# Performance work log

Hardware: AMD Instinct MI355X
Metric: run time of the kernel (lower is better)

Reference implementation:

```python
import jax, jax.numpy as jnp
import numpy as np

P = 399   # number of unshared per-position Conv1d kernels
K = 5     # conv kernel width (padding=2, 'same')


def _conv_stage(x, W, b):
    """Locally-connected stage: a distinct Conv1d per position along the last axis.
    x: [B, Cin, T, P]; W: [P, Cout, Cin, K]; b: [P, Cout] -> [B, Cout, T, P]."""
    xt = jnp.transpose(x, (3, 0, 1, 2))  # [P, B, Cin, T]

    def one(xi, wi, bi):
        y = jax.lax.conv_general_dilated(xi, wi, (1,), [(2, 2)],
                                         dimension_numbers=('NCH', 'OIH', 'NCH'))
        return y + bi[None, :, None]

    y = jax.vmap(one)(xt, W, b)          # [P, B, Cout, T]
    return jnp.transpose(y, (1, 2, 3, 0))


def _maxpool(x):
    # MaxPool2d((10,1), stride=(3,1)) over [B, C, T, P]
    return jax.lax.reduce_window(x, -jnp.inf, jax.lax.max,
                                 (1, 1, 10, 1), (1, 1, 3, 1), 'VALID')


def setup_inputs() -> dict:
    key = jax.random.key(0)
    ks = jax.random.split(key, 32)
    B, T = 256, 365

    def rn(k, shape, scale):
        return jax.random.normal(k, shape, jnp.float32) * scale

    d = {}
    d['x'] = jax.random.normal(ks[0], (B, T, P), jnp.float32)
    d['x2'] = jax.random.normal(ks[1], (B, 1307), jnp.float32)
    # per-position conv weights (PyTorch Conv1d layout O,I,K, stacked over P)
    d['W1'] = rn(ks[2], (P, 3, 1, K), 0.3); d['b1'] = rn(ks[3], (P, 3), 0.05)
    d['W2'] = rn(ks[4], (P, 3, 3, K), 0.2); d['b2'] = rn(ks[5], (P, 3), 0.05)
    d['W3'] = rn(ks[6], (P, 3, 3, K), 0.2); d['b3'] = rn(ks[7], (P, 3), 0.05)
    d['W4'] = rn(ks[8], (P, 3, 3, K), 0.2); d['b4'] = rn(ks[9], (P, 3), 0.05)
    # self.layers: 1307 -> 700 -> 200 -> 100
    d['lW1'] = rn(ks[10], (1307, 700), 0.02); d['lb1'] = rn(ks[11], (700,), 0.01)
    d['lW2'] = rn(ks[12], (700, 200), 0.03);  d['lb2'] = rn(ks[13], (200,), 0.01)
    d['lW3'] = rn(ks[14], (200, 100), 0.05);  d['lb3'] = rn(ks[15], (100,), 0.01)
    # self.common_layers: 1297 -> 500 -> 100 -> 20
    d['cW1'] = rn(ks[16], (1297, 500), 0.02); d['cb1'] = rn(ks[17], (500,), 0.01)
    d['cW2'] = rn(ks[18], (500, 100), 0.04);  d['cb2'] = rn(ks[19], (100,), 0.01)
    d['cW3'] = rn(ks[20], (100, 20), 0.08);   d['cb3'] = rn(ks[21], (20,), 0.01)
    # last_layer: 20 -> 1
    d['fW'] = rn(ks[22], (20, 1), 0.2);       d['fb'] = rn(ks[23], (1,), 0.01)
    return d


def reference(x, x2, W1, b1, W2, b2, W3, b3, W4, b4,
              lW1, lb1, lW2, lb2, lW3, lb3,
              cW1, cb1, cW2, cb2, cW3, cb3, fW, fb):
    h = x[:, None, :, :]                       # [B, 1, T, P]
    for W, b in ((W1, b1), (W2, b2), (W3, b3), (W4, b4)):
        h = _maxpool(jax.nn.relu(_conv_stage(h, W, b)))
    enc1 = h.reshape(h.shape[0], -1)           # [B, 3*1*399] = [B, 1197]

    e = jax.nn.relu(x2 @ lW1 + lb1)
    e = jax.nn.relu(e @ lW2 + lb2)
    enc2 = e @ lW3 + lb3                       # [B, 100] (no ReLU on final Linear)

    c = jnp.concatenate([enc1, enc2], axis=1)  # [B, 1297]
    c = jax.nn.relu(c @ cW1 + cb1)
    c = jax.nn.relu(c @ cW2 + cb2)
    c = jax.nn.relu(c @ cW3 + cb3)
    return c @ fW + fb                         # [B, 1]
```

## Files before the change

kernel.cpp:

```cpp
#include <hip/hip_runtime.h>

#define PP 399
#define BB 256


template<int SEG>
__device__ __forceinline__ float xload(const float* __restrict__ inp, int idx) {
    if (SEG == 2) {
        int ic = idx < 364 ? idx : 364;
        float v = inp[(long)ic * PP];
        return (idx <= 364) ? v : 0.f;
    }
    return inp[(long)idx * PP];
}

template<int OFF>
__device__ __forceinline__ void s1_group(const float (&xv)[13],
    const float (&w1)[3][5], const float (&B1)[3],
    float (&A1)[3], float (&c0)[3])
{
#pragma unroll
    for (int co = 0; co < 3; ++co) {
        float a0 = B1[co], a1 = B1[co], a2 = B1[co];
#pragma unroll
        for (int t = 0; t < 5; ++t) {
            a0 = fmaf(xv[OFF + t],     w1[co][t], a0);
            a1 = fmaf(xv[OFF + 1 + t], w1[co][t], a1);
            a2 = fmaf(xv[OFF + 2 + t], w1[co][t], a2);
        }
        c0[co] = a0;
        A1[co] = fmaxf(fmaxf(a0, a1), a2);
    }
}

template<int P2>
__device__ __forceinline__ void s2_step(
    float (&fe)[3][4], const float (&e)[3],
    const float (&w2)[3][3][5], const float (&B2)[3],
    float (&A2a)[3], float (&A2b)[3], float (&A2c)[3], float (&A2cur)[3],
    float*& op, bool do_c2, bool do_emit)
{
    if (do_c2) {
        float c2v[3];
#pragma unroll
        for (int co = 0; co < 3; ++co) {
            float a = B2[co];
#pragma unroll
            for (int ci = 0; ci < 3; ++ci) {
                a = fmaf(fe[ci][0], w2[co][ci][0], a);
                a = fmaf(fe[ci][1], w2[co][ci][1], a);
                a = fmaf(fe[ci][2], w2[co][ci][2], a);
                a = fmaf(fe[ci][3], w2[co][ci][3], a);
                a = fmaf(e[ci],     w2[co][ci][4], a);
            }
            c2v[co] = a;
        }
        if (P2 == 0) {
#pragma unroll
            for (int co = 0; co < 3; ++co) { A2a[co] = A2b[co]; A2b[co] = A2c[co]; A2c[co] = A2cur[co]; }
            if (do_emit) {
#pragma unroll
                for (int co = 0; co < 3; ++co)
                    op[co * PP] = fmaxf(fmaxf(fmaxf(fmaxf(A2a[co], A2b[co]), A2c[co]), c2v[co]), 0.f);
                op += 3 * PP;
            }
#pragma unroll
            for (int co = 0; co < 3; ++co) A2cur[co] = c2v[co];
        } else {
#pragma unroll
            for (int co = 0; co < 3; ++co) A2cur[co] = fmaxf(A2cur[co], c2v[co]);
        }
    }
#pragma unroll
    for (int ci = 0; ci < 3; ++ci) {
        fe[ci][0] = fe[ci][1]; fe[ci][1] = fe[ci][2]; fe[ci][2] = fe[ci][3]; fe[ci][3] = e[ci];
    }
}

template<int P2>
__device__ __forceinline__ void emit_e(
    const float (&Aa)[3], const float (&Ab)[3], const float (&Ac)[3],
    const float (&c0)[3],
    float (&fe)[3][4],
    const float (&w2)[3][3][5], const float (&B2)[3],
    float (&A2a)[3], float (&A2b)[3], float (&A2c)[3], float (&A2cur)[3],
    float*& op, bool do_c2, bool do_emit)
{
    float e[3];
#pragma unroll
    for (int co = 0; co < 3; ++co)
        e[co] = fmaxf(fmaxf(fmaxf(fmaxf(Aa[co], Ab[co]), Ac[co]), c0[co]), 0.f);
    s2_step<P2>(fe, e, w2, B2, A2a, A2b, A2c, A2cur, op, do_c2, do_emit);
}

template<int SEG>
__device__ __forceinline__ void s12_body(
    const float* __restrict__ x,
    const float* __restrict__ W1, const float* __restrict__ b1,
    const float* __restrict__ W2, const float* __restrict__ b2,
    float* __restrict__ h2, int b, int p)
{
    constexpr int J0tab[4] = {0, 13, 25, 37};
    constexpr int j0 = J0tab[SEG];
    constexpr int j1 = J0tab[SEG + 1];
    constexpr int k0 = (SEG == 0) ? 0 : 3 * j0 - 2;
    constexpr int kend = (3 * j1 + 11 < 121) ? (3 * j1 + 11) : 121;
    constexpr int NGRP = kend - k0 + 1;
    constexpr int NS = NGRP / 3;
    constexpr int NREM = NGRP - 3 * NS;
    constexpr int c2start = (SEG == 0) ? 5 : (k0 + 7);
    constexpr int e2start = 3 * j0 + 14;
    constexpr int P2_0 = (SEG == 0) ? 1 : 2;
    constexpr int P2_1 = (SEG == 0) ? 2 : 0;
    constexpr int P2_2 = (SEG == 0) ? 0 : 1;

    float w1[3][5], B1[3];
    {
        const float* wp = W1 + (long)p * 15;
#pragma unroll
        for (int co = 0; co < 3; ++co) {
#pragma unroll
            for (int t = 0; t < 5; ++t) w1[co][t] = wp[co * 5 + t];
            B1[co] = b1[(long)p * 3 + co];
        }
    }
    float w2[3][3][5], B2[3];
    {
        const float* wp = W2 + (long)p * 45;
#pragma unroll
        for (int co = 0; co < 3; ++co) {
#pragma unroll
            for (int ci = 0; ci < 3; ++ci)
#pragma unroll
                for (int t = 0; t < 5; ++t) w2[co][ci][t] = wp[(co * 3 + ci) * 5 + t];
            B2[co] = b2[(long)p * 3 + co];
        }
    }

    const float* __restrict__ inp = x + (long)b * 365 * PP + p;
    float* op = h2 + ((long)b * 37 + j0) * 3 * PP + p;

    float xv[13];
#pragma unroll
    for (int s = 0; s < 13; ++s) {
        int idx = 3 * k0 - 2 + s;
        xv[s] = (idx >= 0) ? inp[(long)idx * PP] : 0.f;
    }

    float fe[3][4];
    float A1p[3][3];
    float A2a[3], A2b[3], A2c[3], A2cur[3];
#pragma unroll
    for (int ci = 0; ci < 3; ++ci)
#pragma unroll
        for (int s = 0; s < 4; ++s) fe[ci][s] = 0.f;
#pragma unroll
    for (int co = 0; co < 3; ++co) {
        A1p[0][co] = 0.f; A1p[1][co] = 0.f; A1p[2][co] = 0.f;
        A2a[co] = 0.f; A2b[co] = 0.f; A2c[co] = 0.f; A2cur[co] = 0.f;
    }

    for (int S = 0; S < NS; ++S) {
        int k = k0 + 3 * S;
        float q[9];
#pragma unroll
        for (int s = 0; s < 9; ++s)
            q[s] = xload<SEG>(inp, 3 * k + 11 + s);

        float A1c0[3], A1c1[3], A1c2[3], c0[3];

        s1_group<0>(xv, w1, B1, A1c0, c0);
        if (S >= 1)
            emit_e<P2_0>(A1p[0], A1p[1], A1p[2], c0, fe, w2, B2,
                         A2a, A2b, A2c, A2cur, op,
                         k >= c2start, k >= e2start);
        s1_group<3>(xv, w1, B1, A1c1, c0);
        if (S >= 1)
            emit_e<P2_1>(A1p[1], A1p[2], A1c0, c0, fe, w2, B2,
                         A2a, A2b, A2c, A2cur, op,
                         k + 1 >= c2start, k + 1 >= e2start);
        s1_group<6>(xv, w1, B1, A1c2, c0);
        if (S >= 1)
            emit_e<P2_2>(A1p[2], A1c0, A1c1, c0, fe, w2, B2,
                         A2a, A2b, A2c, A2cur, op,
                         k + 2 >= c2start, k + 2 >= e2start);

#pragma unroll
        for (int co = 0; co < 3; ++co) {
            A1p[0][co] = A1c0[co]; A1p[1][co] = A1c1[co]; A1p[2][co] = A1c2[co];
        }
        xv[0] = xv[9]; xv[1] = xv[10]; xv[2] = xv[11]; xv[3] = xv[12];
#pragma unroll
        for (int s = 0; s < 9; ++s) xv[4 + s] = q[s];
    }

    if constexpr (NREM >= 1) {
        int k = k0 + 3 * NS;
        float A1c0[3], c0[3];
        s1_group<0>(xv, w1, B1, A1c0, c0);
        emit_e<P2_0>(A1p[0], A1p[1], A1p[2], c0, fe, w2, B2,
                     A2a, A2b, A2c, A2cur, op,
                     k >= c2start, k >= e2start);
        if constexpr (NREM >= 2) {
            float A1c1[3];
            s1_group<3>(xv, w1, B1, A1c1, c0);
            emit_e<P2_1>(A1p[1], A1p[2], A1c0, c0, fe, w2, B2,
                         A2a, A2b, A2c, A2cur, op,
                         k + 1 >= c2start, k + 1 >= e2start);
        }
    }
    if constexpr (SEG == 2) {
        float ez[3] = {0.f, 0.f, 0.f};
        s2_step<0>(fe, ez, w2, B2, A2a, A2b, A2c, A2cur, op, true, true);
    }
}

template<int RELU_A>
__device__ __forceinline__ void gemm_tile(
    const float* __restrict__ A, const float* __restrict__ Wt,
    float* __restrict__ out, int K, int N, int lda, int ldo, int kchunk,
    int bx, int by, int bz)
{
    __shared__ float As[32][36];
    __shared__ float Bs[32][36];

    int tid = threadIdx.x;
    int ty  = tid >> 3;
    int tx4 = (tid & 7) * 4;
    int c0 = bx * 32;
    int m0 = by * 32;
    int k0 = bz * kchunk;
    int klim = min(K, k0 + kchunk);

    float4 acc = make_float4(0.f, 0.f, 0.f, 0.f);

    for (int kb = k0; kb < klim; kb += 32) {
#pragma unroll
        for (int j = 0; j < 4; ++j) {
            int kk = kb + tx4 + j;
            float v = (kk < klim) ? A[(long)(m0 + ty) * lda + kk] : 0.f;
            if (RELU_A) v = fmaxf(v, 0.f);
            As[ty][tx4 + j] = v;
        }
#pragma unroll
        for (int j = 0; j < 4; ++j) {
            int kk = kb + ty;
            int c = c0 + tx4 + j;
            Bs[ty][tx4 + j] = (kk < klim && c < N) ? Wt[(long)kk * N + c] : 0.f;
        }
        __syncthreads();
#pragma unroll
        for (int kk = 0; kk < 32; ++kk) {
            float a = As[ty][kk];
            float4 bv = *(const float4*)&Bs[kk][tx4];
            acc.x = fmaf(a, bv.x, acc.x);
            acc.y = fmaf(a, bv.y, acc.y);
            acc.z = fmaf(a, bv.z, acc.z);
            acc.w = fmaf(a, bv.w, acc.w);
        }
        __syncthreads();
    }

    long m = m0 + ty;
    if (c0 + tx4 + 0 < N) atomicAdd(&out[m * ldo + c0 + tx4 + 0], acc.x);
    if (c0 + tx4 + 1 < N) atomicAdd(&out[m * ldo + c0 + tx4 + 1], acc.y);
    if (c0 + tx4 + 2 < N) atomicAdd(&out[m * ldo + c0 + tx4 + 2], acc.z);
    if (c0 + tx4 + 3 < N) atomicAdd(&out[m * ldo + c0 + tx4 + 3], acc.w);
}

template<int RELU_A>
__global__ __launch_bounds__(256)
void gemm_atomic(const float* __restrict__ A, const float* __restrict__ Wt,
                 float* __restrict__ out, int K, int N, int lda, int ldo, int kchunk)
{
    gemm_tile<RELU_A>(A, Wt, out, K, N, lda, ldo, kchunk,
                      blockIdx.x, blockIdx.y, blockIdx.z);
}

__global__ __launch_bounds__(256)
void d1_conv_s12_lw1(const float* __restrict__ x,
                     const float* __restrict__ W1, const float* __restrict__ b1,
                     const float* __restrict__ W2, const float* __restrict__ b2,
                     float* __restrict__ h2,
                     const float* __restrict__ x2, const float* __restrict__ lW1,
                     float* __restrict__ e1)
{
    int blk = blockIdx.x;
    if (blk < 1197) {
        int seg = blk / 399;
        int bx  = blk - seg * 399;
        int gid = bx * 256 + threadIdx.x;
        int b = gid / PP;
        int p = gid - b * PP;
        if (seg == 0)      s12_body<0>(x, W1, b1, W2, b2, h2, b, p);
        else if (seg == 1) s12_body<1>(x, W1, b1, W2, b2, h2, b, p);
        else               s12_body<2>(x, W1, b1, W2, b2, h2, b, p);
    } else {
        int g = blk - 1197;
        int gx = g % 22;
        int gy = (g / 22) % 8;
        int gz = g / 176;
        gemm_tile<0>(x2, lW1, e1, 1307, 700, 1307, 700, 256, gx, gy, gz);
    }
}

template<int CIN>
struct Stage {
    float w[3][CIN][5];
    float b[3];
    float xw[CIN][5];
    float m1[3], m2[3], m3[3];
    int nin;
};

__device__ __forceinline__ void init_s3(Stage<3>& s, const float* __restrict__ Wt,
                                        const float* __restrict__ Bs, int p) {
    const float* wp = Wt + (long)p * 45;
#pragma unroll
    for (int co = 0; co < 3; ++co)
#pragma unroll
        for (int ci = 0; ci < 3; ++ci)
#pragma unroll
            for (int k = 0; k < 5; ++k)
                s.w[co][ci][k] = wp[(co * 3 + ci) * 5 + k];
#pragma unroll
    for (int co = 0; co < 3; ++co) s.b[co] = Bs[(long)p * 3 + co];
#pragma unroll
    for (int ci = 0; ci < 3; ++ci)
#pragma unroll
        for (int k = 0; k < 5; ++k) s.xw[ci][k] = 0.f;
#pragma unroll
    for (int co = 0; co < 3; ++co) { s.m1[co] = -1e30f; s.m2[co] = -1e30f; s.m3[co] = -1e30f; }
    s.nin = 0;
}

template<int CIN>
__device__ __forceinline__ bool feed(Stage<CIN>& s, const float* in, float* out) {
#pragma unroll
    for (int ci = 0; ci < CIN; ++ci) {
        s.xw[ci][0] = s.xw[ci][1];
        s.xw[ci][1] = s.xw[ci][2];
        s.xw[ci][2] = s.xw[ci][3];
        s.xw[ci][3] = s.xw[ci][4];
        s.xw[ci][4] = in[ci];
    }
    int t = s.nin - 2;
    s.nin++;
    if (t < 0) return false;

    float c[3];
#pragma unroll
    for (int co = 0; co < 3; ++co) {
        float a = s.b[co];
#pragma unroll
        for (int ci = 0; ci < CIN; ++ci)
#pragma unroll
            for (int k = 0; k < 5; ++k)
                a = fmaf(s.xw[ci][k], s.w[co][ci][k], a);
        c[co] = fmaxf(a, 0.f);
    }

    bool emit = false;
    int ph = t % 3;
    if (ph == 0) {
        if (t >= 9) {
#pragma unroll
            for (int co = 0; co < 3; ++co) out[co] = fmaxf(s.m1[co], c[co]);
            emit = true;
        }
#pragma unroll
        for (int co = 0; co < 3; ++co) {
            float a = fmaxf(s.m2[co], c[co]);
            float bb = fmaxf(s.m3[co], c[co]);
            s.m1[co] = a; s.m2[co] = bb; s.m3[co] = c[co];
        }
    } else {
#pragma unroll
        for (int co = 0; co < 3; ++co) {
            s.m1[co] = fmaxf(s.m1[co], c[co]);
            s.m2[co] = fmaxf(s.m2[co], c[co]);
            s.m3[co] = fmaxf(s.m3[co], c[co]);
        }
    }
    return emit;
}

__device__ __forceinline__ void s34_body(
    const float* __restrict__ h2,
    const float* __restrict__ W3, const float* __restrict__ b3,
    const float* __restrict__ W4, const float* __restrict__ b4,
    float* __restrict__ cbuf, int b, int p)
{
    Stage<3> s3, s4;
    init_s3(s3, W3, b3, p);
    init_s3(s4, W4, b4, p);

    const float* inp = h2 + (long)b * 37 * 3 * PP + p;
    float* o4 = cbuf + (long)b * 1297 + p;

    float v3[3], v4[3];
    float z[3] = {0.f, 0.f, 0.f};

    float r0[3], r1[3], r2[3], r3[3], r4[3];
#pragma unroll
    for (int ci = 0; ci < 3; ++ci) {
        r0[ci] = inp[(long)(0 * 3 + ci) * PP];
        r1[ci] = inp[(long)(1 * 3 + ci) * PP];
        r2[ci] = inp[(long)(2 * 3 + ci) * PP];
        r3[ci] = inp[(long)(3 * 3 + ci) * PP];
        r4[ci] = inp[(long)(4 * 3 + ci) * PP];
    }

    for (int i = 0; i < 39; ++i) {
        float nn[3];
        int i5 = i + 5;
#pragma unroll
        for (int ci = 0; ci < 3; ++ci)
            nn[ci] = (i5 < 37) ? inp[(long)(i5 * 3 + ci) * PP] : 0.f;
        if (feed(s3, r0, v3)) {
            if (feed(s4, v3, v4)) {
#pragma unroll
                for (int co = 0; co < 3; ++co) o4[co * PP] = v4[co];
            }
        }
#pragma unroll
        for (int ci = 0; ci < 3; ++ci) {
            r0[ci] = r1[ci]; r1[ci] = r2[ci]; r2[ci] = r3[ci]; r3[ci] = r4[ci]; r4[ci] = nn[ci];
        }
    }
    for (int r = 0; r < 2; ++r) {
        if (feed(s4, z, v4)) {
#pragma unroll
            for (int co = 0; co < 3; ++co) o4[co * PP] = v4[co];
        }
    }
}

__global__ __launch_bounds__(256)
void d2_conv_s34_lw2(const float* __restrict__ h2,
                     const float* __restrict__ W3, const float* __restrict__ b3,
                     const float* __restrict__ W4, const float* __restrict__ b4,
                     float* __restrict__ cbuf,
                     const float* __restrict__ e1, const float* __restrict__ lW2,
                     float* __restrict__ e2)
{
    int blk = blockIdx.x;
    if (blk < 399) {
        int gid = blk * 256 + threadIdx.x;
        int b = gid / PP;
        int p = gid - b * PP;
        s34_body(h2, W3, b3, W4, b4, cbuf, b, p);
    } else {
        int g = blk - 399;
        int gx = g % 7;
        int gy = (g / 7) % 8;
        int gz = g / 56;
        gemm_tile<1>(e1, lW2, e2, 700, 200, 700, 200, 128, gx, gy, gz);
    }
}

__global__ __launch_bounds__(256)
void init_bias(float* __restrict__ e1, const float* __restrict__ lb1,
               float* __restrict__ e2, const float* __restrict__ lb2,
               float* __restrict__ enc2, const float* __restrict__ lb3,
               float* __restrict__ c1, const float* __restrict__ cb1,
               float* __restrict__ c2, const float* __restrict__ cb2,
               float* __restrict__ c3, const float* __restrict__ cb3)
{
    int idx = blockIdx.x * 256 + threadIdx.x;
    if (idx < BB * 700) { e1[idx] = lb1[idx % 700]; return; }
    idx -= BB * 700;
    if (idx < BB * 200) { e2[idx] = lb2[idx % 200]; return; }
    idx -= BB * 200;
    if (idx < BB * 100) { int m = idx / 100, c = idx % 100; enc2[(long)m * 1297 + c] = lb3[c]; return; }
    idx -= BB * 100;
    if (idx < BB * 500) { c1[idx] = cb1[idx % 500]; return; }
    idx -= BB * 500;
    if (idx < BB * 100) { c2[idx] = cb2[idx % 100]; return; }
    idx -= BB * 100;
    if (idx < BB * 20)  { c3[idx] = cb3[idx % 20]; return; }
}

__global__ __launch_bounds__(64)
void final_kernel(const float* __restrict__ c3,
                  const float* __restrict__ fW,
                  const float* __restrict__ fb,
                  float* __restrict__ out)
{
    int m = blockIdx.x * 64 + threadIdx.x;
    if (m >= BB) return;
    float acc = fb[0];
#pragma unroll
    for (int k = 0; k < 20; ++k)
        acc = fmaf(fmaxf(c3[m * 20 + k], 0.f), fW[k], acc);
    out[m] = acc;
}

extern "C" void kernel_launch(void* const* d_in, const int* in_sizes, int n_in,
                              void* d_out, int out_size, void* d_ws, size_t ws_size,
                              hipStream_t stream)
{
    const float* x   = (const float*)d_in[0];
    const float* x2  = (const float*)d_in[1];
    const float* W1  = (const float*)d_in[2];
    const float* b1  = (const float*)d_in[3];
    const float* W2  = (const float*)d_in[4];
    const float* b2  = (const float*)d_in[5];
    const float* W3  = (const float*)d_in[6];
    const float* b3  = (const float*)d_in[7];
    const float* W4  = (const float*)d_in[8];
    const float* b4  = (const float*)d_in[9];
    const float* lW1 = (const float*)d_in[10];
    const float* lb1 = (const float*)d_in[11];
    const float* lW2 = (const float*)d_in[12];
    const float* lb2 = (const float*)d_in[13];
    const float* lW3 = (const float*)d_in[14];
    const float* lb3 = (const float*)d_in[15];
    const float* cW1 = (const float*)d_in[16];
    const float* cb1 = (const float*)d_in[17];
    const float* cW2 = (const float*)d_in[18];
    const float* cb2 = (const float*)d_in[19];
    const float* cW3 = (const float*)d_in[20];
    const float* cb3 = (const float*)d_in[21];
    const float* fW  = (const float*)d_in[22];
    const float* fb  = (const float*)d_in[23];
    float* out = (float*)d_out;

    float* ws = (float*)d_ws;
    const long n_h2   = (long)BB * 37 * 3 * PP;
    const long n_cbuf = (long)BB * 1297;
    float* h2   = ws;
    float* cbuf = h2 + n_h2;
    float* e1   = cbuf + n_cbuf;
    float* e2   = e1 + (long)BB * 700;
    float* c1   = e2 + (long)BB * 200;
    float* c2   = c1 + (long)BB * 500;
    float* c3b  = c2 + (long)BB * 100;

    init_bias<<<1620, 256, 0, stream>>>(e1, lb1, e2, lb2, cbuf + 1197, lb3,
                                        c1, cb1, c2, cb2, c3b, cb3);

    d1_conv_s12_lw1<<<1197 + 1056, 256, 0, stream>>>(x, W1, b1, W2, b2, h2,
                                                     x2, lW1, e1);
    d2_conv_s34_lw2<<<399 + 336, 256, 0, stream>>>(h2, W3, b3, W4, b4, cbuf,
                                                   e1, lW2, e2);
    gemm_atomic<1><<<dim3(4, 8, 4), 256, 0, stream>>>(e2, lW3, cbuf + 1197, 200, 100, 200, 1297, 64);

    gemm_atomic<0><<<dim3(16, 8, 6), 256, 0, stream>>>(cbuf, cW1, c1, 1297, 500, 1297, 500, 256);
    gemm_atomic<1><<<dim3( 4, 8, 8), 256, 0, stream>>>(c1, cW2, c2, 500, 100, 500, 100, 64);
    gemm_atomic<1><<<dim3( 1, 8, 4), 256, 0, stream>>>(c2, cW3, c3b, 100, 20, 100, 20, 32);

    final_kernel<<<dim3(4), 64, 0, stream>>>(c3b, fW, fb, out);
}
```

Baseline: 161.6 us.

## Process two batch rows per thread and split conv stages into six time segments

The fused stage-1/2 conv kernel now has each thread handle two batch samples (b and b+128), so the per-position weights loaded into registers are reused across two independent streams and there is more instruction-level parallelism. The time axis is split into six segments instead of three, which keeps the block count roughly the same (1200 vs 1197). The cost is roughly double the register pressure for the per-thread state, which may reduce occupancy or cause spills, plus more halo recomputation at the extra segment boundaries.

```diff
diff --git a/kernel.cpp b/kernel.cpp
--- a/kernel.cpp
+++ b/kernel.cpp
@@ -6,7 +6,7 @@
 
 template<int SEG>
 __device__ __forceinline__ float xload(const float* __restrict__ inp, int idx) {
-    if (SEG == 2) {
+    if (SEG == 5) {
         int ic = idx < 364 ? idx : 364;
         float v = inp[(long)ic * PP];
         return (idx <= 364) ? v : 0.f;
@@ -15,92 +15,112 @@
 }
 
 template<int OFF>
-__device__ __forceinline__ void s1_group(const float (&xv)[13],
+__device__ __forceinline__ void s1g2(const float (&xv)[2][13],
     const float (&w1)[3][5], const float (&B1)[3],
-    float (&A1)[3], float (&c0)[3])
-{
-#pragma unroll
-    for (int co = 0; co < 3; ++co) {
-        float a0 = B1[co], a1 = B1[co], a2 = B1[co];
-#pragma unroll
-        for (int t = 0; t < 5; ++t) {
-            a0 = fmaf(xv[OFF + t],     w1[co][t], a0);
-            a1 = fmaf(xv[OFF + 1 + t], w1[co][t], a1);
-            a2 = fmaf(xv[OFF + 2 + t], w1[co][t], a2);
-        }
-        c0[co] = a0;
-        A1[co] = fmaxf(fmaxf(a0, a1), a2);
-    }
+    float (&A1)[2][3], float (&c0)[2][3])
+{
+#pragma unroll
+    for (int st = 0; st < 2; ++st)
+#pragma unroll
+        for (int co = 0; co < 3; ++co) {
+            float a0 = B1[co], a1 = B1[co], a2 = B1[co];
+#pragma unroll
+            for (int t = 0; t < 5; ++t) {
+                a0 = fmaf(xv[st][OFF + t],     w1[co][t], a0);
+                a1 = fmaf(xv[st][OFF + 1 + t], w1[co][t], a1);
+                a2 = fmaf(xv[st][OFF + 2 + t], w1[co][t], a2);
+            }
+            c0[st][co] = a0;
+            A1[st][co] = fmaxf(fmaxf(a0, a1), a2);
+        }
 }
 
 template<int P2>
-__device__ __forceinline__ void s2_step(
-    float (&fe)[3][4], const float (&e)[3],
+__device__ __forceinline__ void s2s2(
+    float (&fe)[2][3][4], const float (&e)[2][3],
     const float (&w2)[3][3][5], const float (&B2)[3],
-    float (&A2a)[3], float (&A2b)[3], float (&A2c)[3], float (&A2cur)[3],
-    float*& op, bool do_c2, bool do_emit)
+    float (&A2a)[2][3], float (&A2b)[2][3], float (&A2c)[2][3], float (&A2cur)[2][3],
+    float* (&op)[2], bool do_c2, bool do_emit)
 {
     if (do_c2) {
-        float c2v[3];
-#pragma unroll
-        for (int co = 0; co < 3; ++co) {
-            float a = B2[co];
-#pragma unroll
-            for (int ci = 0; ci < 3; ++ci) {
-                a = fmaf(fe[ci][0], w2[co][ci][0], a);
-                a = fmaf(fe[ci][1], w2[co][ci][1], a);
-                a = fmaf(fe[ci][2], w2[co][ci][2], a);
-                a = fmaf(fe[ci][3], w2[co][ci][3], a);
-                a = fmaf(e[ci],     w2[co][ci][4], a);
+        float c2v[2][3];
+#pragma unroll
+        for (int st = 0; st < 2; ++st)
+#pragma unroll
+            for (int co = 0; co < 3; ++co) {
+                float a = B2[co];
+#pragma unroll
+                for (int ci = 0; ci < 3; ++ci) {
+                    a = fmaf(fe[st][ci][0], w2[co][ci][0], a);
+                    a = fmaf(fe[st][ci][1], w2[co][ci][1], a);
+                    a = fmaf(fe[st][ci][2], w2[co][ci][2], a);
+                    a = fmaf(fe[st][ci][3], w2[co][ci][3], a);
+                    a = fmaf(e[st][ci],     w2[co][ci][4], a);
+                }
+                c2v[st][co] = a;
             }
-            c2v[co] = a;
-        }
         if (P2 == 0) {
 #pragma unroll
-            for (int co = 0; co < 3; ++co) { A2a[co] = A2b[co]; A2b[co] = A2c[co]; A2c[co] = A2cur[co]; }
+            for (int st = 0; st < 2; ++st)
+#pragma unroll
+                for (int co = 0; co < 3; ++co) {
+                    A2a[st][co] = A2b[st][co]; A2b[st][co] = A2c[st][co]; A2c[st][co] = A2cur[st][co];
+                }
             if (do_emit) {
 #pragma unroll
-                for (int co = 0; co < 3; ++co)
-                    op[co * PP] = fmaxf(fmaxf(fmaxf(fmaxf(A2a[co], A2b[co]), A2c[co]), c2v[co]), 0.f);
-                op += 3 * PP;
+                for (int st = 0; st < 2; ++st) {
+#pragma unroll
+                    for (int co = 0; co < 3; ++co)
+                        op[st][co * PP] = fmaxf(fmaxf(fmaxf(fmaxf(A2a[st][co], A2b[st][co]), A2c[st][co]), c2v[st][co]), 0.f);
+                    op[st] += 3 * PP;
+                }
             }
 #pragma unroll
-            for (int co = 0; co < 3; ++co) A2cur[co] = c2v[co];
+            for (int st = 0; st < 2; ++st)
+#pragma unroll
+                for (int co = 0; co < 3; ++co) A2cur[st][co] = c2v[st][co];
         } else {
 #pragma unroll
-            for (int co = 0; co < 3; ++co) A2cur[co] = fmaxf(A2cur[co], c2v[co]);
-        }
-    }
-#pragma unroll
-    for (int ci = 0; ci < 3; ++ci) {
-        fe[ci][0] = fe[ci][1]; fe[ci][1] = fe[ci][2]; fe[ci][2] = fe[ci][3]; fe[ci][3] = e[ci];
-    }
+            for (int st = 0; st < 2; ++st)
+#pragma unroll
+                for (int co = 0; co < 3; ++co) A2cur[st][co] = fmaxf(A2cur[st][co], c2v[st][co]);
+        }
+    }
+#pragma unroll
+    for (int st = 0; st < 2; ++st)
+#pragma unroll
+        for (int ci = 0; ci < 3; ++ci) {
+            fe[st][ci][0] = fe[st][ci][1]; fe[st][ci][1] = fe[st][ci][2];
+            fe[st][ci][2] = fe[st][ci][3]; fe[st][ci][3] = e[st][ci];
+        }
 }
 
 template<int P2>
-__device__ __forceinline__ void emit_e(
-    const float (&Aa)[3], const float (&Ab)[3], const float (&Ac)[3],
-    const float (&c0)[3],
-    float (&fe)[3][4],
+__device__ __forceinline__ void emit2(
+    const float (&Aa)[2][3], const float (&Ab)[2][3], const float (&Ac)[2][3],
+    const float (&c0)[2][3],
+    float (&fe)[2][3][4],
     const float (&w2)[3][3][5], const float (&B2)[3],
-    float (&A2a)[3], float (&A2b)[3], float (&A2c)[3], float (&A2cur)[3],
-    float*& op, bool do_c2, bool do_emit)
-{
-    float e[3];
-#pragma unroll
-    for (int co = 0; co < 3; ++co)
-        e[co] = fmaxf(fmaxf(fmaxf(fmaxf(Aa[co], Ab[co]), Ac[co]), c0[co]), 0.f);
-    s2_step<P2>(fe, e, w2, B2, A2a, A2b, A2c, A2cur, op, do_c2, do_emit);
+    float (&A2a)[2][3], float (&A2b)[2][3], float (&A2c)[2][3], float (&A2cur)[2][3],
+    float* (&op)[2], bool do_c2, bool do_emit)
+{
+    float e[2][3];
+#pragma unroll
+    for (int st = 0; st < 2; ++st)
+#pragma unroll
+        for (int co = 0; co < 3; ++co)
+            e[st][co] = fmaxf(fmaxf(fmaxf(fmaxf(Aa[st][co], Ab[st][co]), Ac[st][co]), c0[st][co]), 0.f);
+    s2s2<P2>(fe, e, w2, B2, A2a, A2b, A2c, A2cur, op, do_c2, do_emit);
 }
 
 template<int SEG>
-__device__ __forceinline__ void s12_body(
+__device__ __forceinline__ void s12_dual(
     const float* __restrict__ x,
     const float* __restrict__ W1, const float* __restrict__ b1,
     const float* __restrict__ W2, const float* __restrict__ b2,
     float* __restrict__ h2, int b, int p)
 {
-    constexpr int J0tab[4] = {0, 13, 25, 37};
+    constexpr int J0tab[7] = {0, 7, 13, 19, 25, 31, 37};
     constexpr int j0 = J0tab[SEG];
     constexpr int j1 = J0tab[SEG + 1];
     constexpr int k0 = (SEG == 0) ? 0 : 3 * j0 - 2;
@@ -137,81 +157,94 @@
         }
     }
 
-    const float* __restrict__ inp = x + (long)b * 365 * PP + p;
-    float* op = h2 + ((long)b * 37 + j0) * 3 * PP + p;
-
-    float xv[13];
-#pragma unroll
-    for (int s = 0; s < 13; ++s) {
-        int idx = 3 * k0 - 2 + s;
-        xv[s] = (idx >= 0) ? inp[(long)idx * PP] : 0.f;
-    }
-
-    float fe[3][4];
-    float A1p[3][3];
-    float A2a[3], A2b[3], A2c[3], A2cur[3];
-#pragma unroll
-    for (int ci = 0; ci < 3; ++ci)
-#pragma unroll
-        for (int s = 0; s < 4; ++s) fe[ci][s] = 0.f;
-#pragma unroll
-    for (int co = 0; co < 3; ++co) {
-        A1p[0][co] = 0.f; A1p[1][co] = 0.f; A1p[2][co] = 0.f;
-        A2a[co] = 0.f; A2b[co] = 0.f; A2c[co] = 0.f; A2cur[co] = 0.f;
+    const float* inp[2] = { x + (long)b * 365 * PP + p,
+                            x + (long)(b + 128) * 365 * PP + p };
+    float* op[2] = { h2 + ((long)b * 37 + j0) * 3 * PP + p,
+                     h2 + ((long)(b + 128) * 37 + j0) * 3 * PP + p };
+
+    float xv[2][13];
+#pragma unroll
+    for (int st = 0; st < 2; ++st)
+#pragma unroll
+        for (int s = 0; s < 13; ++s) {
+            int idx = 3 * k0 - 2 + s;
+            xv[st][s] = (idx >= 0) ? inp[st][(long)idx * PP] : 0.f;
+        }
+
+    float fe[2][3][4];
+    float A1p0[2][3], A1p1[2][3], A1p2[2][3];
+    float A2a[2][3], A2b[2][3], A2c[2][3], A2cur[2][3];
+#pragma unroll
+    for (int st = 0; st < 2; ++st) {
+#pragma unroll
+        for (int ci = 0; ci < 3; ++ci)
+#pragma unroll
+            for (int s = 0; s < 4; ++s) fe[st][ci][s] = 0.f;
+#pragma unroll
+        for (int co = 0; co < 3; ++co) {
+            A1p0[st][co] = 0.f; A1p1[st][co] = 0.f; A1p2[st][co] = 0.f;
+            A2a[st][co] = 0.f; A2b[st][co] = 0.f; A2c[st][co] = 0.f; A2cur[st][co] = 0.f;
+        }
     }
 
     for (int S = 0; S < NS; ++S) {
         int k = k0 + 3 * S;
-        float q[9];
-#pragma unroll
-        for (int s = 0; s < 9; ++s)
-            q[s] = xload<SEG>(inp, 3 * k + 11 + s);
-
-        float A1c0[3], A1c1[3], A1c2[3], c0[3];
-
-        s1_group<0>(xv, w1, B1, A1c0, c0);
+        float q[2][9];
+#pragma unroll
+        for (int st = 0; st < 2; ++st)
+#pragma unroll
+            for (int s = 0; s < 9; ++s)
+                q[st][s] = xload<SEG>(inp[st], 3 * k + 11 + s);
+
+        float A1c0[2][3], A1c1[2][3], A1c2[2][3], c0[2][3];
+
+        s1g2<0>(xv, w1, B1, A1c0, c0);
         if (S >= 1)
-            emit_e<P2_0>(A1p[0], A1p[1], A1p[2], c0, fe, w2, B2,
-                         A2a, A2b, A2c, A2cur, op,
-                         k >= c2start, k >= e2start);
-        s1_group<3>(xv, w1, B1, A1c1, c0);
+            emit2<P2_0>(A1p0, A1p1, A1p2, c0, fe, w2, B2,
+                        A2a, A2b, A2c, A2cur, op,
+                        k >= c2start, k >= e2start);
+        s1g2<3>(xv, w1, B1, A1c1, c0);
         if (S >= 1)
-            emit_e<P2_1>(A1p[1], A1p[2], A1c0, c0, fe, w2, B2,
-                         A2a, A2b, A2c, A2cur, op,
-                         k + 1 >= c2start, k + 1 >= e2start);
-        s1_group<6>(xv, w1, B1, A1c2, c0);
+            emit2<P2_1>(A1p1, A1p2, A1c0, c0, fe, w2, B2,
+                        A2a, A2b, A2c, A2cur, op,
+                        k + 1 >= c2start, k + 1 >= e2start);
+        s1g2<6>(xv, w1, B1, A1c2, c0);
         if (S >= 1)
-            emit_e<P2_2>(A1p[2], A1c0, A1c1, c0, fe, w2, B2,
-                         A2a, A2b, A2c, A2cur, op,
-                         k + 2 >= c2start, k + 2 >= e2start);
-
-#pragma unroll
-        for (int co = 0; co < 3; ++co) {
-            A1p[0][co] = A1c0[co]; A1p[1][co] = A1c1[co]; A1p[2][co] = A1c2[co];
-        }
-        xv[0] = xv[9]; xv[1] = xv[10]; xv[2] = xv[11]; xv[3] = xv[12];
-#pragma unroll
-        for (int s = 0; s < 9; ++s) xv[4 + s] = q[s];
+            emit2<P2_2>(A1p2, A1c0, A1c1, c0, fe, w2, B2,
+                        A2a, A2b, A2c, A2cur, op,
+                        k + 2 >= c2start, k + 2 >= e2start);
+
+#pragma unroll
+        for (int st = 0; st < 2; ++st) {
+#pragma unroll
+            for (int co = 0; co < 3; ++co) {
+                A1p0[st][co] = A1c0[st][co]; A1p1[st][co] = A1c1[st][co]; A1p2[st][co] = A1c2[st][co];
+            }
+            xv[st][0] = xv[st][9]; xv[st][1] = xv[st][10];
+            xv[st][2] = xv[st][11]; xv[st][3] = xv[st][12];
+#pragma unroll
+            for (int s = 0; s < 9; ++s) xv[st][4 + s] = q[st][s];
+        }
     }
 
     if constexpr (NREM >= 1) {
         int k = k0 + 3 * NS;
-        float A1c0[3], c0[3];
-        s1_group<0>(xv, w1, B1, A1c0, c0);
-        emit_e<P2_0>(A1p[0], A1p[1], A1p[2], c0, fe, w2, B2,
-                     A2a, A2b, A2c, A2cur, op,
-                     k >= c2start, k >= e2start);
+        float A1c0[2][3], c0[2][3];
+        s1g2<0>(xv, w1, B1, A1c0, c0);
+        emit2<P2_0>(A1p0, A1p1, A1p2, c0, fe, w2, B2,
+                    A2a, A2b, A2c, A2cur, op,
+                    k >= c2start, k >= e2start);
         if constexpr (NREM >= 2) {
-            float A1c1[3];
-            s1_group<3>(xv, w1, B1, A1c1, c0);
-            emit_e<P2_1>(A1p[1], A1p[2], A1c0, c0, fe, w2, B2,
-                         A2a, A2b, A2c, A2cur, op,
-                         k + 1 >= c2start, k + 1 >= e2start);
-        }
-    }
-    if constexpr (SEG == 2) {
-        float ez[3] = {0.f, 0.f, 0.f};
-        s2_step<0>(fe, ez, w2, B2, A2a, A2b, A2c, A2cur, op, true, true);
+            float A1c1[2][3];
+            s1g2<3>(xv, w1, B1, A1c1, c0);
+            emit2<P2_1>(A1p1, A1p2, A1c0, c0, fe, w2, B2,
+                        A2a, A2b, A2c, A2cur, op,
+                        k + 1 >= c2start, k + 1 >= e2start);
+        }
+    }
+    if constexpr (SEG == 5) {
+        float ez[2][3] = {{0.f, 0.f, 0.f}, {0.f, 0.f, 0.f}};
+        s2s2<0>(fe, ez, w2, B2, A2a, A2b, A2c, A2cur, op, true, true);
     }
 }
 
@@ -286,17 +319,23 @@
                      float* __restrict__ e1)
 {
     int blk = blockIdx.x;
-    if (blk < 1197) {
-        int seg = blk / 399;
-        int bx  = blk - seg * 399;
+    if (blk < 1200) {
+        int seg = blk / 200;
+        int bx  = blk - seg * 200;
         int gid = bx * 256 + threadIdx.x;
+        if (gid >= 128 * PP) return;
         int b = gid / PP;
         int p = gid - b * PP;
-        if (seg == 0)      s12_body<0>(x, W1, b1, W2, b2, h2, b, p);
-        else if (seg == 1) s12_body<1>(x, W1, b1, W2, b2, h2, b, p);
-        else               s12_body<2>(x, W1, b1, W2, b2, h2, b, p);
+        switch (seg) {
+            case 0: s12_dual<0>(x, W1, b1, W2, b2, h2, b, p); break;
+            case 1: s12_dual<1>(x, W1, b1, W2, b2, h2, b, p); break;
+            case 2: s12_dual<2>(x, W1, b1, W2, b2, h2, b, p); break;
+            case 3: s12_dual<3>(x, W1, b1, W2, b2, h2, b, p); break;
+            case 4: s12_dual<4>(x, W1, b1, W2, b2, h2, b, p); break;
+            default: s12_dual<5>(x, W1, b1, W2, b2, h2, b, p); break;
+        }
     } else {
-        int g = blk - 1197;
+        int g = blk - 1200;
         int gx = g % 22;
         int gy = (g / 22) % 8;
         int gz = g / 176;
@@ -540,7 +579,7 @@
     init_bias<<<1620, 256, 0, stream>>>(e1, lb1, e2, lb2, cbuf + 1197, lb3,
                                         c1, cb1, c2, cb2, c3b, cb3);
 
-    d1_conv_s12_lw1<<<1197 + 1056, 256, 0, stream>>>(x, W1, b1, W2, b2, h2,
+    d1_conv_s12_lw1<<<1200 + 1056, 256, 0, stream>>>(x, W1, b1, W2, b2, h2,
                                                      x2, lW1, e1);
     d2_conv_s34_lw2<<<399 + 336, 256, 0, stream>>>(h2, W3, b3, W4, b4, cbuf,
                                                    e1, lW2, e2);
```

New measurement: 228.7 us. +41.6%, slower.

## Fold bias init into conv launch and overlap cW1 enc1 part with lW3 GEMM

Applied to the files above, without the earlier changes.

Only e1's bias init stays as a standalone kernel; the other bias buffers are now filled by extra blocks appended to the first conv/GEMM launch. The cW1 GEMM is split by K range: its enc1 part (first 1197 rows) runs in the same launch as the lW3 GEMM, since it does not depend on enc2. A small follow-up launch then handles the remaining 100 rows that come from enc2. The aim is to shorten the serial chain of small kernels and fill the GPU better, at the cost of more complex block dispatch.

```diff
diff --git a/kernel.cpp b/kernel.cpp
--- a/kernel.cpp
+++ b/kernel.cpp
@@ -278,12 +278,24 @@
 }
 
 __global__ __launch_bounds__(256)
+void init_e1(float* __restrict__ e1, const float* __restrict__ lb1)
+{
+    int idx = blockIdx.x * 256 + threadIdx.x;
+    if (idx < BB * 700) e1[idx] = lb1[idx % 700];
+}
+
+__global__ __launch_bounds__(256)
 void d1_conv_s12_lw1(const float* __restrict__ x,
                      const float* __restrict__ W1, const float* __restrict__ b1,
                      const float* __restrict__ W2, const float* __restrict__ b2,
                      float* __restrict__ h2,
                      const float* __restrict__ x2, const float* __restrict__ lW1,
-                     float* __restrict__ e1)
+                     float* __restrict__ e1,
+                     float* __restrict__ e2,  const float* __restrict__ lb2,
+                     float* __restrict__ cbuf, const float* __restrict__ lb3,
+                     float* __restrict__ c1,  const float* __restrict__ cb1,
+                     float* __restrict__ c2,  const float* __restrict__ cb2,
+                     float* __restrict__ c3b, const float* __restrict__ cb3)
 {
     int blk = blockIdx.x;
     if (blk < 1197) {
@@ -295,12 +307,23 @@
         if (seg == 0)      s12_body<0>(x, W1, b1, W2, b2, h2, b, p);
         else if (seg == 1) s12_body<1>(x, W1, b1, W2, b2, h2, b, p);
         else               s12_body<2>(x, W1, b1, W2, b2, h2, b, p);
-    } else {
+    } else if (blk < 1197 + 1056) {
         int g = blk - 1197;
         int gx = g % 22;
         int gy = (g / 22) % 8;
         int gz = g / 176;
         gemm_tile<0>(x2, lW1, e1, 1307, 700, 1307, 700, 256, gx, gy, gz);
+    } else {
+        int idx = (blk - 2253) * 256 + threadIdx.x;
+        if (idx < BB * 200) { e2[idx] = lb2[idx % 200]; return; }
+        idx -= BB * 200;
+        if (idx < BB * 100) { int m = idx / 100, c = idx % 100; cbuf[(long)m * 1297 + 1197 + c] = lb3[c]; return; }
+        idx -= BB * 100;
+        if (idx < BB * 500) { c1[idx] = cb1[idx % 500]; return; }
+        idx -= BB * 500;
+        if (idx < BB * 100) { c2[idx] = cb2[idx % 100]; return; }
+        idx -= BB * 100;
+        if (idx < BB * 20)  { c3b[idx] = cb3[idx % 20]; return; }
     }
 }
 
@@ -460,25 +483,23 @@
 }
 
 __global__ __launch_bounds__(256)
-void init_bias(float* __restrict__ e1, const float* __restrict__ lb1,
-               float* __restrict__ e2, const float* __restrict__ lb2,
-               float* __restrict__ enc2, const float* __restrict__ lb3,
-               float* __restrict__ c1, const float* __restrict__ cb1,
-               float* __restrict__ c2, const float* __restrict__ cb2,
-               float* __restrict__ c3, const float* __restrict__ cb3)
-{
-    int idx = blockIdx.x * 256 + threadIdx.x;
-    if (idx < BB * 700) { e1[idx] = lb1[idx % 700]; return; }
-    idx -= BB * 700;
-    if (idx < BB * 200) { e2[idx] = lb2[idx % 200]; return; }
-    idx -= BB * 200;
-    if (idx < BB * 100) { int m = idx / 100, c = idx % 100; enc2[(long)m * 1297 + c] = lb3[c]; return; }
-    idx -= BB * 100;
-    if (idx < BB * 500) { c1[idx] = cb1[idx % 500]; return; }
-    idx -= BB * 500;
-    if (idx < BB * 100) { c2[idx] = cb2[idx % 100]; return; }
-    idx -= BB * 100;
-    if (idx < BB * 20)  { c3[idx] = cb3[idx % 20]; return; }
+void d3_lw3_cw1a(const float* __restrict__ e2, const float* __restrict__ lW3,
+                 float* __restrict__ cbuf,
+                 const float* __restrict__ cW1, float* __restrict__ c1)
+{
+    int blk = blockIdx.x;
+    if (blk < 128) {
+        int gx = blk % 4;
+        int gy = (blk / 4) % 8;
+        int gz = blk / 32;
+        gemm_tile<1>(e2, lW3, cbuf + 1197, 200, 100, 200, 1297, 64, gx, gy, gz);
+    } else {
+        int g = blk - 128;
+        int gx = g % 16;
+        int gy = (g / 16) % 8;
+        int gz = g / 128;
+        gemm_tile<0>(cbuf, cW1, c1, 1197, 500, 1297, 500, 200, gx, gy, gz);
+    }
 }
 
 __global__ __launch_bounds__(64)
@@ -537,16 +558,19 @@
     float* c2   = c1 + (long)BB * 500;
     float* c3b  = c2 + (long)BB * 100;
 
-    init_bias<<<1620, 256, 0, stream>>>(e1, lb1, e2, lb2, cbuf + 1197, lb3,
-                                        c1, cb1, c2, cb2, c3b, cb3);
-
-    d1_conv_s12_lw1<<<1197 + 1056, 256, 0, stream>>>(x, W1, b1, W2, b2, h2,
-                                                     x2, lW1, e1);
+    init_e1<<<700, 256, 0, stream>>>(e1, lb1);
+
+    d1_conv_s12_lw1<<<1197 + 1056 + 920, 256, 0, stream>>>(
+        x, W1, b1, W2, b2, h2, x2, lW1, e1,
+        e2, lb2, cbuf, lb3, c1, cb1, c2, cb2, c3b, cb3);
+
     d2_conv_s34_lw2<<<399 + 336, 256, 0, stream>>>(h2, W3, b3, W4, b4, cbuf,
                                                    e1, lW2, e2);
-    gemm_atomic<1><<<dim3(4, 8, 4), 256, 0, stream>>>(e2, lW3, cbuf + 1197, 200, 100, 200, 1297, 64);
-
-    gemm_atomic<0><<<dim3(16, 8, 6), 256, 0, stream>>>(cbuf, cW1, c1, 1297, 500, 1297, 500, 256);
+
+    d3_lw3_cw1a<<<128 + 768, 256, 0, stream>>>(e2, lW3, cbuf, cW1, c1);
+
+    gemm_atomic<0><<<dim3(16, 8, 1), 256, 0, stream>>>(cbuf + 1197, cW1 + (long)1197 * 500, c1, 100, 500, 1297, 500, 100);
+
     gemm_atomic<1><<<dim3( 4, 8, 8), 256, 0, stream>>>(c1, cW2, c2, 500, 100, 500, 100, 64);
     gemm_atomic<1><<<dim3( 1, 8, 4), 256, 0, stream>>>(c2, cW3, c3b, 100, 20, 100, 20, 32);
 
```

Result: no change. 164.4 us (+1.7%).
